# Kernel optimization log

Measured on AMD Instinct MI355X. Metric: run time of the kernel, lower is better.

## Reference

```python
import jax, jax.numpy as jnp
import numpy as np

SIZE = 64      # base glimpse height/width
DEPTH = 3
SCALE = 2


def _bilinear_glimpse(img, ys, xs):
    """Bilinear sample img [B,H,W,C] on an axis-aligned grid.
    ys: [B,hd] fractional row coords, xs: [B,wd] fractional col coords.
    Out-of-bounds samples are zero (glimpse padding). Returns [B,hd,wd,C]."""
    B, H, W, C = img.shape
    y0 = jnp.floor(ys).astype(jnp.int32)
    x0 = jnp.floor(xs).astype(jnp.int32)
    wy = (ys - y0.astype(ys.dtype))[:, :, None, None]   # [B,hd,1,1]
    wx = (xs - x0.astype(xs.dtype))[:, None, :, None]   # [B,1,wd,1]
    bidx = jnp.arange(B)[:, None, None]

    def gather(yi, xi):
        my = (yi >= 0) & (yi < H)
        mx = (xi >= 0) & (xi < W)
        yc = jnp.clip(yi, 0, H - 1)
        xc = jnp.clip(xi, 0, W - 1)
        v = img[bidx, yc[:, :, None], xc[:, None, :], :]          # [B,hd,wd,C]
        m = (my[:, :, None] & mx[:, None, :])[..., None]
        return jnp.where(m, v, jnp.zeros((), img.dtype))

    return (gather(y0, x0) * (1 - wy) * (1 - wx)
            + gather(y0, x0 + 1) * (1 - wy) * wx
            + gather(y0 + 1, x0) * wy * (1 - wx)
            + gather(y0 + 1, x0 + 1) * wy * wx)


def setup_inputs() -> dict:
    key = jax.random.key(0)
    k1, k2 = jax.random.split(key)
    inputs = jax.random.normal(k1, (64, 512, 512, 3), dtype=jnp.float32)
    # normalized centered offsets in [-0.5, 0.5] so all scales stay mostly in-bounds
    offsets = jax.random.uniform(k2, (64, 2), dtype=jnp.float32, minval=-0.5, maxval=0.5)
    return {"inputs": inputs, "offsets": offsets}


def reference(inputs, offsets):
    B, H, W, C = inputs.shape
    h = w = SIZE
    # tf.image.extract_glimpse centered+normalized: center pixel = (off+1)*dim/2
    cy = (offsets[:, 0] + 1.0) * (H / 2.0)   # [B]
    cx = (offsets[:, 1] + 1.0) * (W / 2.0)
    outs = []
    for d in range(DEPTH):
        k = SCALE ** d
        hd, wd = h * k, w * k
        ys = cy[:, None] + (jnp.arange(hd, dtype=jnp.float32) - (hd - 1) / 2.0)
        xs = cx[:, None] + (jnp.arange(wd, dtype=jnp.float32) - (wd - 1) / 2.0)
        g = _bilinear_glimpse(inputs, ys, xs)                    # [B,hd,wd,C]
        if d > 0:  # avg_pool ksize=stride=k, VALID -> back to [B,h,w,C]
            g = g.reshape(B, h, k, w, k, C).mean(axis=(2, 4))
        outs.append(g)
    out = jnp.stack(outs, axis=4)            # [B,h,w,C,depth]
    return out.reshape(B, h, w, C * DEPTH)
```

## Files before the change

kernel.cpp:

```cpp
#include <hip/hip_runtime.h>

#define OSZ 64
#define NB  64
#define IH  512
#define IW  512
#define NC  3
#define ND  3

template<int K>
__device__ __forceinline__ void glimpse_eval(const float* __restrict__ img,
                                             int b, int y, int x,
                                             float cy, float cx,
                                             float* __restrict__ out3) {
    const float halfspan = (float)(OSZ * K - 1) * 0.5f;
    float ybase = cy + ((float)(y * K) - halfspan);
    float xbase = cx + ((float)(x * K) - halfspan);
    float y0f = floorf(ybase), x0f = floorf(xbase);
    float fy = ybase - y0f, fx = xbase - x0f;
    int y0 = (int)y0f, x0 = (int)x0f;

    float wx[K + 1];
    wx[0] = 1.0f - fx;
#pragma unroll
    for (int s = 1; s < K; ++s) wx[s] = 1.0f;
    wx[K] = fx;
#pragma unroll
    for (int s = 0; s <= K; ++s) {
        int xi = x0 + s;
        if (xi < 0 || xi >= IW) wx[s] = 0.0f;
    }

    float a0 = 0.f, a1 = 0.f, a2 = 0.f;
#pragma unroll
    for (int r = 0; r <= K; ++r) {
        int yi = y0 + r;
        float wy = (r == 0) ? (1.0f - fy) : ((r == K) ? fy : 1.0f);
        if (yi < 0 || yi >= IH) continue;
        const float* rowp = img + ((size_t)b * IH + (size_t)yi) * (IW * NC);
        float r0 = 0.f, r1 = 0.f, r2 = 0.f;
#pragma unroll
        for (int s = 0; s <= K; ++s) {
            int xi = x0 + s;
            int xc = xi < 0 ? 0 : (xi >= IW ? IW - 1 : xi);
            const float* p = rowp + xc * NC;
            float w = wx[s];
            r0 += w * p[0];
            r1 += w * p[1];
            r2 += w * p[2];
        }
        a0 += wy * r0; a1 += wy * r1; a2 += wy * r2;
    }
    const float inv = 1.0f / (float)(K * K);
    out3[0] = a0 * inv; out3[1] = a1 * inv; out3[2] = a2 * inv;
}

__global__ __launch_bounds__(256)
void SpatialGlimpse_kernel(const float* __restrict__ img,
                           const float* __restrict__ off,
                           float* __restrict__ out) {
    int idx = blockIdx.x * 256 + threadIdx.x;
    int x = idx & 63;
    int y = (idx >> 6) & 63;
    int b = (idx >> 12) & 63;
    int d = idx >> 18;

    float cy = (off[2 * b + 0] + 1.0f) * ((float)IH * 0.5f);
    float cx = (off[2 * b + 1] + 1.0f) * ((float)IW * 0.5f);

    float v[3];
    if (d == 0)      glimpse_eval<1>(img, b, y, x, cy, cx, v);
    else if (d == 1) glimpse_eval<2>(img, b, y, x, cy, cx, v);
    else             glimpse_eval<4>(img, b, y, x, cy, cx, v);

    size_t o = (((size_t)b * OSZ + y) * OSZ + x) * (NC * ND) + d;
    out[o]          = v[0];
    out[o + ND]     = v[1];
    out[o + 2 * ND] = v[2];
}

extern "C" void kernel_launch(void* const* d_in, const int* in_sizes, int n_in,
                              void* d_out, int out_size, void* d_ws, size_t ws_size,
                              hipStream_t stream) {
    const float* img = (const float*)d_in[0];
    const float* off = (const float*)d_in[1];
    float* out = (float*)d_out;

    const int total = ND * NB * OSZ * OSZ;
    const int block = 256;
    const int grid = total / block;
    SpatialGlimpse_kernel<<<grid, block, 0, stream>>>(img, off, out);
}
```

Before: 254.0 us.

## Stage glimpse source tiles in LDS with per-depth row tiling

Each block now cooperatively loads the needed image window for a band of output rows into shared memory as channel-planar, swizzled arrays, then computes bilinear/pooled outputs from LDS with each thread handling several rows. The grid is restructured per depth (1, 4, or 16 tiles per batch) instead of one thread per output. This is meant to remove redundant uncoalesced global loads of overlapping pixels, at the cost of a large LDS footprint that limits occupancy, and very few blocks (1344) for the depth-0 and depth-1 cases.

```diff
diff --git a/kernel.cpp b/kernel.cpp
--- a/kernel.cpp
+++ b/kernel.cpp
@@ -7,17 +7,48 @@
 #define NC  3
 #define ND  3
 
-template<int K>
-__device__ __forceinline__ void glimpse_eval(const float* __restrict__ img,
-                                             int b, int y, int x,
-                                             float cy, float cx,
-                                             float* __restrict__ out3) {
+#define LDS_FLOATS (3 * 19 * 268)
+
+__device__ __forceinline__ int swz(int p) { return p + (p >> 5); }
+
+template<int K, int R>
+__device__ __forceinline__ void glimpse_tile(const float* __restrict__ img,
+                                             float* __restrict__ out,
+                                             float* __restrict__ lds,
+                                             int b, int tile, int d,
+                                             float cy, float cx) {
+    constexpr int ROWS  = R * K + 3;
+    constexpr int COLS  = OSZ * K + 3;
+    constexpr int PITCH = COLS + (COLS >> 5) + 1;
+    constexpr int PLANE = ROWS * PITCH;
     const float halfspan = (float)(OSZ * K - 1) * 0.5f;
-    float ybase = cy + ((float)(y * K) - halfspan);
+    const int tid = threadIdx.x;
+    const int yfirst = tile * R;
+
+    float yb0 = cy + ((float)(yfirst * K) - halfspan);
+    float xb0 = cx + (0.0f - halfspan);
+    int ry0 = (int)floorf(yb0) - 1;
+    int rx0 = (int)floorf(xb0) - 1;
+
+    for (int lin = tid; lin < ROWS * COLS; lin += 256) {
+        int r = lin / COLS;
+        int p = lin - r * COLS;
+        int gy = ry0 + r; gy = gy < 0 ? 0 : (gy > IH - 1 ? IH - 1 : gy);
+        int gx = rx0 + p; gx = gx < 0 ? 0 : (gx > IW - 1 ? IW - 1 : gx);
+        const float* src = img + (((size_t)b * IH + gy) * IW + gx) * NC;
+        int a = r * PITCH + swz(p);
+        lds[a]             = src[0];
+        lds[PLANE + a]     = src[1];
+        lds[2 * PLANE + a] = src[2];
+    }
+    __syncthreads();
+
+    int x = tid & 63;
     float xbase = cx + ((float)(x * K) - halfspan);
-    float y0f = floorf(ybase), x0f = floorf(xbase);
-    float fy = ybase - y0f, fx = xbase - x0f;
-    int y0 = (int)y0f, x0 = (int)x0f;
+    float x0f = floorf(xbase);
+    float fx = xbase - x0f;
+    int x0 = (int)x0f;
+    int ix = x0 - rx0;
 
     float wx[K + 1];
     wx[0] = 1.0f - fx;
@@ -30,52 +61,58 @@
         if (xi < 0 || xi >= IW) wx[s] = 0.0f;
     }
 
-    float a0 = 0.f, a1 = 0.f, a2 = 0.f;
+    const float inv = 1.0f / (float)(K * K);
 #pragma unroll
-    for (int r = 0; r <= K; ++r) {
-        int yi = y0 + r;
-        float wy = (r == 0) ? (1.0f - fy) : ((r == K) ? fy : 1.0f);
-        if (yi < 0 || yi >= IH) continue;
-        const float* rowp = img + ((size_t)b * IH + (size_t)yi) * (IW * NC);
-        float r0 = 0.f, r1 = 0.f, r2 = 0.f;
+    for (int j = 0; j < R / 4; ++j) {
+        int y = yfirst + (tid >> 6) + j * 4;
+        float ybase = cy + ((float)(y * K) - halfspan);
+        float y0f = floorf(ybase);
+        float fy = ybase - y0f;
+        int y0 = (int)y0f;
+        int iy = y0 - ry0;
+
+        float a0 = 0.f, a1 = 0.f, a2 = 0.f;
 #pragma unroll
-        for (int s = 0; s <= K; ++s) {
-            int xi = x0 + s;
-            int xc = xi < 0 ? 0 : (xi >= IW ? IW - 1 : xi);
-            const float* p = rowp + xc * NC;
-            float w = wx[s];
-            r0 += w * p[0];
-            r1 += w * p[1];
-            r2 += w * p[2];
+        for (int r = 0; r <= K; ++r) {
+            int yi = y0 + r;
+            float wy = (r == 0) ? (1.0f - fy) : ((r == K) ? fy : 1.0f);
+            if (yi < 0 || yi >= IH) continue;
+            const float* p0 = lds + (iy + r) * PITCH;
+            float r0 = 0.f, r1 = 0.f, r2 = 0.f;
+#pragma unroll
+            for (int s = 0; s <= K; ++s) {
+                float w = wx[s];
+                int a = swz(ix + s);
+                r0 += w * p0[a];
+                r1 += w * p0[PLANE + a];
+                r2 += w * p0[2 * PLANE + a];
+            }
+            a0 += wy * r0; a1 += wy * r1; a2 += wy * r2;
         }
-        a0 += wy * r0; a1 += wy * r1; a2 += wy * r2;
+        size_t o = (((size_t)b * OSZ + y) * OSZ + x) * (NC * ND) + d;
+        out[o]          = a0 * inv;
+        out[o + ND]     = a1 * inv;
+        out[o + 2 * ND] = a2 * inv;
     }
-    const float inv = 1.0f / (float)(K * K);
-    out3[0] = a0 * inv; out3[1] = a1 * inv; out3[2] = a2 * inv;
 }
 
 __global__ __launch_bounds__(256)
 void SpatialGlimpse_kernel(const float* __restrict__ img,
                            const float* __restrict__ off,
                            float* __restrict__ out) {
-    int idx = blockIdx.x * 256 + threadIdx.x;
-    int x = idx & 63;
-    int y = (idx >> 6) & 63;
-    int b = (idx >> 12) & 63;
-    int d = idx >> 18;
+    __shared__ float lds[LDS_FLOATS];
+    int bid = blockIdx.x;
+    int d, b, tile;
+    if (bid < NB)               { d = 0; b = bid;            tile = 0; }
+    else if (bid < NB + NB * 4) { int t = bid - NB;     d = 1; b = t >> 2; tile = t & 3; }
+    else                        { int t = bid - NB * 5; d = 2; b = t >> 4; tile = t & 15; }
 
     float cy = (off[2 * b + 0] + 1.0f) * ((float)IH * 0.5f);
     float cx = (off[2 * b + 1] + 1.0f) * ((float)IW * 0.5f);
 
-    float v[3];
-    if (d == 0)      glimpse_eval<1>(img, b, y, x, cy, cx, v);
-    else if (d == 1) glimpse_eval<2>(img, b, y, x, cy, cx, v);
-    else             glimpse_eval<4>(img, b, y, x, cy, cx, v);
-
-    size_t o = (((size_t)b * OSZ + y) * OSZ + x) * (NC * ND) + d;
-    out[o]          = v[0];
-    out[o + ND]     = v[1];
-    out[o + 2 * ND] = v[2];
+    if (d == 0)      glimpse_tile<1, 64>(img, out, lds, b, tile, 0, cy, cx);
+    else if (d == 1) glimpse_tile<2, 16>(img, out, lds, b, tile, 1, cy, cx);
+    else             glimpse_tile<4, 4>(img, out, lds, b, tile, 2, cy, cx);
 }
 
 extern "C" void kernel_launch(void* const* d_in, const int* in_sizes, int n_in,
@@ -85,8 +122,6 @@
     const float* off = (const float*)d_in[1];
     float* out = (float*)d_out;
 
-    const int total = ND * NB * OSZ * OSZ;
-    const int block = 256;
-    const int grid = total / block;
-    SpatialGlimpse_kernel<<<grid, block, 0, stream>>>(img, off, out);
+    const int grid = NB + NB * 4 + NB * 16;
+    SpatialGlimpse_kernel<<<grid, 256, 0, stream>>>(img, off, out);
 }
```

Result: slower. 270.5 us (+6.5%).
